# Optimization experiments

Measured on AMD Instinct MI355X. Metric: run time of the kernel, lower is better.

Reference implementation:

```python
import jax, jax.numpy as jnp
import numpy as np

MEMORY_SIZE = 32768
FEATURE_DIM = 128
BATCH = 4096


def setup_inputs() -> dict:
    key = jax.random.key(0)
    k1, k2, k3, k4 = jax.random.split(key, 4)
    memory = jax.random.normal(k1, (MEMORY_SIZE, FEATURE_DIM), dtype=jnp.float32)
    input_data = jax.random.normal(k2, (BATCH, FEATURE_DIM), dtype=jnp.float32)
    write_weights = jax.random.uniform(k3, (BATCH, MEMORY_SIZE), dtype=jnp.float32)
    query = jax.random.normal(k4, (BATCH, FEATURE_DIM), dtype=jnp.float32)
    return {"memory": memory, "input_data": input_data,
            "write_weights": write_weights, "query": query}


def reference(memory, input_data, write_weights, query):
    # ---- write(): row-normalize weights, scatter-accumulate into memory ----
    # The original python double-loop computes update[j] += w[i,j] * x[i],
    # i.e. update = w_norm.T @ x  -- a single GEMM.
    w_norm = write_weights / jnp.sum(write_weights, axis=1, keepdims=True)
    update = jnp.einsum('bm,bf->mf', w_norm, input_data)  # [M, F]
    memory_new = memory + update

    # ---- read(): softmax attention over memory slots ----
    scores = jnp.matmul(query, memory_new.T)              # [B, M]
    attention_weights = jax.nn.softmax(scores, axis=1)
    retrieved_memory = jnp.matmul(attention_weights, memory_new)  # [B, F]
    confidence_scores = jnp.max(attention_weights, axis=1)        # [B]
    return retrieved_memory, confidence_scores, memory_new
```

## Files before the change

kernel.cpp:

```cpp
#include <hip/hip_runtime.h>
#include <hip/hip_bf16.h>
#include <math.h>

#define MEMSZ 32768
#define FDIM  128
#define BATCH 4096

typedef float f32x4 __attribute__((ext_vector_type(4)));
typedef _Float16 f16x8 __attribute__((ext_vector_type(8)));
typedef short bf16x8 __attribute__((ext_vector_type(8)));
typedef unsigned short u16t;
typedef unsigned int u32t;

static __device__ __forceinline__ u16t f2h_bits(float f) {
    union { _Float16 h; u16t u; } c;
    c.h = (_Float16)f;
    return c.u;
}

#define GLDS16(gsrc, ldst) \
  __builtin_amdgcn_global_load_lds((const __attribute__((address_space(1))) void*)(gsrc), \
                                   (__attribute__((address_space(3))) void*)(ldst), 16, 0, 0)

__global__ __launch_bounds__(256) void k_sumT(const float* __restrict__ W,
                                              float* __restrict__ partial,
                                              unsigned char* __restrict__ WT64) {
    __shared__ __align__(16) unsigned char xs[32768];
    const int tid = threadIdx.x;
    const int bt = blockIdx.x & 63, mt = blockIdx.x >> 6;

    #pragma unroll
    for (int i = 0; i < 8; ++i) {
        const int gi = tid + i * 256;
        const int b = gi >> 5;
        const int srcoff = ((gi & 31) * 16) ^ ((b & 7) << 4);
        GLDS16((const unsigned char*)W + ((size_t)(bt * 64 + b) * MEMSZ + (size_t)mt * 128) * 4 + srcoff,
               &xs[gi * 16]);
    }
    asm volatile("s_waitcnt vmcnt(0)" ::: "memory");
    __syncthreads();

    {
        const int b = tid >> 2, q = tid & 3;
        float s = 0.f;
        #pragma unroll
        for (int j = 0; j < 8; ++j) {
            const int off = b * 512 + ((q * 128 + j * 16) ^ ((b & 7) << 4));
            const float4 v = *reinterpret_cast<const float4*>(&xs[off]);
            s += (v.x + v.y) + (v.z + v.w);
        }
        s += __shfl_xor(s, 1);
        s += __shfl_xor(s, 2);
        if (q == 0) partial[(size_t)mt * BATCH + bt * 64 + b] = s;
    }

    unsigned char* dst = WT64 + ((size_t)mt * 64 + bt) * 16384;
    #pragma unroll
    for (int k = 0; k < 4; ++k) {
        const int ci = tid + k * 256;
        const int wm = ci >> 8, mf = (ci >> 7) & 1, ks = (ci >> 6) & 1;
        const int l6 = ci & 63, g = l6 >> 4, q16 = l6 & 15;
        const int m = wm * 32 + mf * 16 + q16;
        u32t pk[4];
        #pragma unroll
        for (int h = 0; h < 4; ++h) {
            const int b0 = ks * 32 + g * 8 + 2 * h;
            const float lo = *reinterpret_cast<const float*>(
                &xs[b0 * 512 + ((m * 4) ^ ((b0 & 7) << 4))]);
            const float hi = *reinterpret_cast<const float*>(
                &xs[(b0 + 1) * 512 + ((m * 4) ^ (((b0 + 1) & 7) << 4))]);
            asm("v_cvt_pk_bf16_f32 %0, %1, %2" : "=v"(pk[h]) : "v"(lo), "v"(hi));
        }
        *reinterpret_cast<uint4*>(dst + ci * 16) = make_uint4(pk[0], pk[1], pk[2], pk[3]);
    }
}

__global__ __launch_bounds__(256) void k_inv(const float* __restrict__ partial,
                                             float* __restrict__ inv_s) {
    const int b = blockIdx.x * 256 + threadIdx.x;
    float s0 = 0.f, s1 = 0.f, s2 = 0.f, s3 = 0.f;
    for (int mt = 0; mt < 256; mt += 4) {
        s0 += partial[(size_t)mt * BATCH + b];
        s1 += partial[(size_t)(mt + 1) * BATCH + b];
        s2 += partial[(size_t)(mt + 2) * BATCH + b];
        s3 += partial[(size_t)(mt + 3) * BATCH + b];
    }
    inv_s[b] = 1.0f / ((s0 + s1) + (s2 + s3));
}

__global__ __launch_bounds__(256) void k_prep(const float* __restrict__ X,
                                              const float* __restrict__ inv_s,
                                              unsigned char* __restrict__ XT64) {
    __shared__ float xs[64][132];
    const int T = blockIdx.x;
    const int b0 = T * 64;
    const int tid = threadIdx.x;
    #pragma unroll
    for (int i = 0; i < 8; ++i) {
        const int idx = tid + i * 256;
        const int row = idx >> 5, c4 = idx & 31;
        const float s = inv_s[b0 + row];
        float4 v = *reinterpret_cast<const float4*>(&X[(size_t)(b0 + row) * FDIM + c4 * 4]);
        v.x *= s; v.y *= s; v.z *= s; v.w *= s;
        *reinterpret_cast<float4*>(&xs[row][c4 * 4]) = v;
    }
    __syncthreads();
    #pragma unroll
    for (int i = 0; i < 4; ++i) {
        const int L = tid + i * 256;
        const int fh = L >> 9, ff = (L >> 7) & 3, ks = (L >> 6) & 1, ln = L & 63;
        const int f = fh * 64 + ff * 16 + (ln & 15);
        const int bi = ks * 32 + (ln >> 4) * 8;
        u32t pk[4];
        #pragma unroll
        for (int h = 0; h < 4; ++h) {
            const float lo = xs[bi + 2 * h][f];
            const float hi = xs[bi + 2 * h + 1][f];
            asm("v_cvt_pk_bf16_f32 %0, %1, %2" : "=v"(pk[h]) : "v"(lo), "v"(hi));
        }
        *reinterpret_cast<uint4*>(XT64 + (size_t)T * 16384 + (size_t)L * 16) =
            make_uint4(pk[0], pk[1], pk[2], pk[3]);
    }
}

__global__ __launch_bounds__(512, 2) void k_update_mfma2(
    const unsigned char* __restrict__ WT64, const unsigned char* __restrict__ XT64,
    const float* __restrict__ Mem, float* __restrict__ MemNew,
    u16t* __restrict__ MemH, u16t* __restrict__ MemHT)
{
    const int tid = threadIdx.x;
    const int lane = tid & 63, w = tid >> 6;
    const int q16 = lane & 15, g = lane >> 4;
    const int wm = w >> 1, wf = w & 1;
    const int mblk = blockIdx.x * 128;

    const unsigned char* wbase = WT64 + (size_t)blockIdx.x * (64 * 16384)
                               + (size_t)(wm * 4096 + lane * 16);
    const unsigned char* xbase = XT64 + (size_t)(wf * 8192 + lane * 16);

    f32x4 acc[2][4];
    #pragma unroll
    for (int mf = 0; mf < 2; ++mf)
        #pragma unroll
        for (int ff = 0; ff < 4; ++ff) acc[mf][ff] = (f32x4){0.f, 0.f, 0.f, 0.f};

    auto issue = [&](bf16x8 (&ar)[2][2], bf16x8 (&br)[4][2], int t) {
        const unsigned char* wp = wbase + (size_t)t * 16384;
        #pragma unroll
        for (int mf = 0; mf < 2; ++mf)
            #pragma unroll
            for (int ks = 0; ks < 2; ++ks)
                ar[mf][ks] = *reinterpret_cast<const bf16x8*>(wp + mf * 2048 + ks * 1024);
        const unsigned char* xp = xbase + (size_t)t * 16384;
        #pragma unroll
        for (int ff = 0; ff < 4; ++ff)
            #pragma unroll
            for (int ks = 0; ks < 2; ++ks)
                br[ff][ks] = *reinterpret_cast<const bf16x8*>(xp + ff * 2048 + ks * 1024);
    };
    auto compute = [&](bf16x8 (&ar)[2][2], bf16x8 (&br)[4][2]) {
        #pragma unroll
        for (int mf = 0; mf < 2; ++mf)
            #pragma unroll
            for (int ff = 0; ff < 4; ++ff)
                #pragma unroll
                for (int ks = 0; ks < 2; ++ks)
                    acc[mf][ff] = __builtin_amdgcn_mfma_f32_16x16x32_bf16(
                        ar[mf][ks], br[ff][ks], acc[mf][ff], 0, 0, 0);
    };

    bf16x8 aE[2][2], bE[4][2], aO[2][2], bO[4][2];
    issue(aE, bE, 0); issue(aO, bO, 1);
    const int NT = BATCH / 64;
    for (int t = 0; t < NT; t += 2) {
        compute(aE, bE);
        if (t + 2 < NT) issue(aE, bE, t + 2);
        compute(aO, bO);
        if (t + 3 < NT) issue(aO, bO, t + 3);
    }

    #pragma unroll
    for (int mf = 0; mf < 2; ++mf) {
        #pragma unroll
        for (int ff = 0; ff < 4; ++ff) {
            const int m0 = mblk + wm * 32 + mf * 16 + g * 4;
            const int fcol = wf * 64 + ff * 16 + q16;
            ushort4 ht;
            u16t* htp = reinterpret_cast<u16t*>(&ht);
            #pragma unroll
            for (int r = 0; r < 4; ++r) {
                const size_t idx = (size_t)(m0 + r) * FDIM + fcol;
                const float v = acc[mf][ff][r] + Mem[idx];
                MemNew[idx] = v;
                const u16t hb = f2h_bits(v);
                MemH[idx] = hb;
                htp[r] = hb;
            }
            *reinterpret_cast<ushort4*>(&MemHT[(size_t)fcol * MEMSZ + m0]) = ht;
        }
    }
}

__global__ __launch_bounds__(256) void k_attn_mfma(
    const float* __restrict__ Q, const u16t* __restrict__ Kh, const u16t* __restrict__ KhT,
    float* __restrict__ accP, float* __restrict__ mP, float* __restrict__ lP, int s_shift)
{
    __shared__ __align__(16) unsigned char kv_u8[2][16384];
    __shared__ __align__(16) unsigned char v_u8[2][16384];
    __shared__ __align__(16) unsigned char p_u8[4][2048];

    const int tid = threadIdx.x;
    const int w = tid >> 6, lane = tid & 63;
    const int q16 = lane & 15, g = lane >> 4;
    const int S = 1 << s_shift;
    const int s_idx = blockIdx.x & (S - 1);
    const int qb = blockIdx.x >> s_shift;
    const int chunk = MEMSZ >> s_shift;
    const int slot0 = s_idx * chunk;
    const int NT = chunk >> 6;

    f16x8 qfrag[2][4];
    #pragma unroll
    for (int qf = 0; qf < 2; ++qf) {
        const float* qrow = Q + (size_t)(qb * 128 + w * 32 + qf * 16 + q16) * FDIM;
        #pragma unroll
        for (int ks = 0; ks < 4; ++ks) {
            float tmp[8];
            *reinterpret_cast<float4*>(&tmp[0]) = *reinterpret_cast<const float4*>(&qrow[ks * 32 + g * 8]);
            *reinterpret_cast<float4*>(&tmp[4]) = *reinterpret_cast<const float4*>(&qrow[ks * 32 + g * 8 + 4]);
            f16x8 v;
            #pragma unroll
            for (int e = 0; e < 8; ++e) v[e] = (_Float16)tmp[e];
            qfrag[qf][ks] = v;
        }
    }

    auto stage = [&](int buf, int tile) {
        const unsigned char* kbase = (const unsigned char*)Kh + (size_t)(slot0 + tile * 64) * 256;
        const unsigned char* tbase = (const unsigned char*)KhT + (size_t)(slot0 + tile * 64) * 2;
        #pragma unroll
        for (int c = 0; c < 4; ++c) {
            const int C = w * 4 + c;
            const int pp = C * 1024 + lane * 16;
            {
                const int slot = pp >> 8;
                const int inner = (pp & 255) ^ ((slot & 7) << 4);
                GLDS16(kbase + slot * 256 + inner, &kv_u8[buf][C * 1024]);
            }
            {
                const int d = pp >> 7;
                const int inner = (pp & 127) ^ ((d & 7) << 4);
                GLDS16(tbase + (size_t)d * 65536 + inner, &v_u8[buf][C * 1024]);
            }
        }
    };

    float m_run[2] = {-3.0e38f, -3.0e38f};
    float l_run[2] = {0.f, 0.f};
    f32x4 acc_o[8][2];
    #pragma unroll
    for (int df = 0; df < 8; ++df)
        #pragma unroll
        for (int qf = 0; qf < 2; ++qf)
            acc_o[df][qf] = (f32x4){0.f, 0.f, 0.f, 0.f};

    stage(0, 0);
    asm volatile("s_waitcnt vmcnt(0)" ::: "memory");
    __builtin_amdgcn_s_barrier();
    __builtin_amdgcn_sched_barrier(0);

    int cur = 0;
    for (int t = 0; t < NT; ++t) {
        if (t + 1 < NT) stage(cur ^ 1, t + 1);

        f32x4 acc_s[4][2];
        #pragma unroll
        for (int sf = 0; sf < 4; ++sf) {
            acc_s[sf][0] = (f32x4){0.f, 0.f, 0.f, 0.f};
            acc_s[sf][1] = (f32x4){0.f, 0.f, 0.f, 0.f};
        }
        const unsigned char* kvb = &kv_u8[cur][0];
        #pragma unroll
        for (int ks = 0; ks < 4; ++ks) {
            #pragma unroll
            for (int sf = 0; sf < 4; ++sf) {
                const int slot = sf * 16 + q16;
                const f16x8 a = *reinterpret_cast<const f16x8*>(
                    kvb + slot * 256 + ((ks * 64 + g * 16) ^ ((slot & 7) << 4)));
                acc_s[sf][0] = __builtin_amdgcn_mfma_f32_16x16x32_f16(a, qfrag[0][ks], acc_s[sf][0], 0, 0, 0);
                acc_s[sf][1] = __builtin_amdgcn_mfma_f32_16x16x32_f16(a, qfrag[1][ks], acc_s[sf][1], 0, 0, 0);
            }
        }

        f16x8 pb[2][2];
        unsigned char* pw = &p_u8[w][0];
        #pragma unroll
        for (int qf = 0; qf < 2; ++qf) {
            float pmax = acc_s[0][qf][0];
            #pragma unroll
            for (int sf = 0; sf < 4; ++sf)
                #pragma unroll
                for (int r = 0; r < 4; ++r)
                    pmax = fmaxf(pmax, acc_s[sf][qf][r]);
            pmax = fmaxf(pmax, __shfl_xor(pmax, 16));
            pmax = fmaxf(pmax, __shfl_xor(pmax, 32));
            const float mn = fmaxf(m_run[qf], pmax);
            float p[4][4];
            float psum = 0.f;
            #pragma unroll
            for (int sf = 0; sf < 4; ++sf)
                #pragma unroll
                for (int r = 0; r < 4; ++r) {
                    p[sf][r] = __expf(acc_s[sf][qf][r] - mn);
                    psum += p[sf][r];
                }
            psum += __shfl_xor(psum, 16);
            psum += __shfl_xor(psum, 32);
            const float sc = __expf(m_run[qf] - mn);
            l_run[qf] = l_run[qf] * sc + psum;
            m_run[qf] = mn;
            #pragma unroll
            for (int df = 0; df < 8; ++df) {
                acc_o[df][qf][0] *= sc; acc_o[df][qf][1] *= sc;
                acc_o[df][qf][2] *= sc; acc_o[df][qf][3] *= sc;
            }
            #pragma unroll
            for (int sf = 0; sf < 4; ++sf)
                #pragma unroll
                for (int rr = 0; rr < 2; ++rr) {
                    const u32t val = (u32t)f2h_bits(p[sf][2 * rr]) | ((u32t)f2h_bits(p[sf][2 * rr + 1]) << 16);
                    const int byte = q16 * 128 + (((sf * 16 + g * 4 + 2 * rr) * 2) ^ ((q16 & 7) << 4));
                    *reinterpret_cast<u32t*>(pw + byte) = val;
                }
            #pragma unroll
            for (int kk = 0; kk < 2; ++kk) {
                const int byte = q16 * 128 + (((kk * 32 + g * 8) * 2) ^ ((q16 & 7) << 4));
                pb[qf][kk] = *reinterpret_cast<const f16x8*>(pw + byte);
            }
        }

        const unsigned char* vb = &v_u8[cur][0];
        #pragma unroll
        for (int df = 0; df < 8; ++df) {
            #pragma unroll
            for (int kk = 0; kk < 2; ++kk) {
                const int d = df * 16 + q16;
                const f16x8 av = *reinterpret_cast<const f16x8*>(
                    vb + d * 128 + ((kk * 64 + g * 16) ^ ((d & 7) << 4)));
                acc_o[df][0] = __builtin_amdgcn_mfma_f32_16x16x32_f16(av, pb[0][kk], acc_o[df][0], 0, 0, 0);
                acc_o[df][1] = __builtin_amdgcn_mfma_f32_16x16x32_f16(av, pb[1][kk], acc_o[df][1], 0, 0, 0);
            }
        }

        asm volatile("s_waitcnt vmcnt(0)" ::: "memory");
        __builtin_amdgcn_s_barrier();
        __builtin_amdgcn_sched_barrier(0);
        cur ^= 1;
    }

    const int rowbase = qb * 128 + w * 32;
    #pragma unroll
    for (int qf = 0; qf < 2; ++qf) {
        const int row = rowbase + qf * 16 + q16;
        float* ap = accP + ((size_t)s_idx * BATCH + row) * FDIM;
        #pragma unroll
        for (int df = 0; df < 8; ++df) {
            float4 o = {acc_o[df][qf][0], acc_o[df][qf][1], acc_o[df][qf][2], acc_o[df][qf][3]};
            *reinterpret_cast<float4*>(&ap[df * 16 + g * 4]) = o;
        }
        if (g == 0) {
            mP[(size_t)s_idx * BATCH + row] = m_run[qf];
            lP[(size_t)s_idx * BATCH + row] = l_run[qf];
        }
    }
}

__global__ __launch_bounds__(256) void k_combine(const float* __restrict__ mP,
                                                 const float* __restrict__ lP,
                                                 const float* __restrict__ accP,
                                                 float* __restrict__ Out,
                                                 float* __restrict__ Conf, int S) {
    const int row = blockIdx.x * 8 + (threadIdx.x >> 5);
    const int lane = threadIdx.x & 31;
    float mt = -3.0e38f;
    for (int s = 0; s < S; ++s) mt = fmaxf(mt, mP[(size_t)s * BATCH + row]);
    float lt = 0.f;
    for (int s = 0; s < S; ++s) lt += lP[(size_t)s * BATCH + row] * __expf(mP[(size_t)s * BATCH + row] - mt);
    const float inv = 1.0f / lt;
    float4 o = {0.f, 0.f, 0.f, 0.f};
    for (int s = 0; s < S; ++s) {
        const float wgt = __expf(mP[(size_t)s * BATCH + row] - mt);
        const float4 a = *reinterpret_cast<const float4*>(&accP[((size_t)s * BATCH + row) * FDIM + lane * 4]);
        o.x += wgt * a.x; o.y += wgt * a.y; o.z += wgt * a.z; o.w += wgt * a.w;
    }
    float4 res = {o.x * inv, o.y * inv, o.z * inv, o.w * inv};
    *reinterpret_cast<float4*>(&Out[(size_t)row * FDIM + lane * 4]) = res;
    if (lane == 0) Conf[row] = inv;
}

__global__ __launch_bounds__(256) void k_rowsum(const float* __restrict__ W,
                                                float* __restrict__ inv_s) {
    const int row = blockIdx.x;
    const float4* Wr = reinterpret_cast<const float4*>(W + (size_t)row * MEMSZ);
    float acc = 0.f;
    #pragma unroll 4
    for (int i = threadIdx.x; i < MEMSZ / 4; i += 256) {
        float4 v = Wr[i];
        acc += (v.x + v.y) + (v.z + v.w);
    }
    #pragma unroll
    for (int off = 32; off > 0; off >>= 1)
        acc += __shfl_down(acc, off, 64);
    __shared__ float wsum[4];
    const int lane = threadIdx.x & 63, wid = threadIdx.x >> 6;
    if (lane == 0) wsum[wid] = acc;
    __syncthreads();
    if (threadIdx.x == 0)
        inv_s[row] = 1.0f / (wsum[0] + wsum[1] + wsum[2] + wsum[3]);
}

#define K2_IT 16
#define K2_MT 64
__global__ __launch_bounds__(256) void k_update_f32(const float* __restrict__ W,
                                                    const float* __restrict__ X,
                                                    const float* __restrict__ inv_s,
                                                    const float* __restrict__ Mem,
                                                    float* __restrict__ MemNew) {
    __shared__ float w_lds[2][K2_IT][K2_MT];
    __shared__ float x_lds[2][K2_IT][FDIM];
    const int j0 = blockIdx.x * K2_MT;
    const int tid = threadIdx.x;
    const int tf = tid & 15;
    const int tj = tid >> 4;

    float acc[4][8];
    #pragma unroll
    for (int a = 0; a < 4; ++a)
        #pragma unroll
        for (int b = 0; b < 8; ++b) acc[a][b] = 0.f;

    float4 pw, px0, px1;
    float ps0, ps1;
    const int wr = tid >> 4, wc4 = tid & 15;
    const int xr0 = tid >> 5, xc0 = tid & 31;
    const int xr1 = (tid + 256) >> 5, xc1 = tid & 31;

    auto load_tile = [&](int it) {
        const int i0 = it * K2_IT;
        pw  = *reinterpret_cast<const float4*>(&W[(size_t)(i0 + wr) * MEMSZ + j0 + wc4 * 4]);
        px0 = *reinterpret_cast<const float4*>(&X[(size_t)(i0 + xr0) * FDIM + xc0 * 4]);
        ps0 = inv_s[i0 + xr0];
        px1 = *reinterpret_cast<const float4*>(&X[(size_t)(i0 + xr1) * FDIM + xc1 * 4]);
        ps1 = inv_s[i0 + xr1];
    };
    auto write_tile = [&](int buf) {
        *reinterpret_cast<float4*>(&w_lds[buf][wr][wc4 * 4]) = pw;
        float4 v = px0; v.x *= ps0; v.y *= ps0; v.z *= ps0; v.w *= ps0;
        *reinterpret_cast<float4*>(&x_lds[buf][xr0][xc0 * 4]) = v;
        float4 u = px1; u.x *= ps1; u.y *= ps1; u.z *= ps1; u.w *= ps1;
        *reinterpret_cast<float4*>(&x_lds[buf][xr1][xc1 * 4]) = u;
    };

    load_tile(0);
    write_tile(0);
    __syncthreads();
    const int NT = BATCH / K2_IT;
    for (int it = 0; it < NT; ++it) {
        const int cur = it & 1;
        if (it + 1 < NT) load_tile(it + 1);
        #pragma unroll 4
        for (int i = 0; i < K2_IT; ++i) {
            const float4 wv = *reinterpret_cast<const float4*>(&w_lds[cur][i][tj * 4]);
            const float4 xa = *reinterpret_cast<const float4*>(&x_lds[cur][i][tf * 4]);
            const float4 xb = *reinterpret_cast<const float4*>(&x_lds[cur][i][tf * 4 + 64]);
            const float wj[4] = {wv.x, wv.y, wv.z, wv.w};
            #pragma unroll
            for (int a = 0; a < 4; ++a) {
                acc[a][0] += wj[a] * xa.x; acc[a][1] += wj[a] * xa.y;
                acc[a][2] += wj[a] * xa.z; acc[a][3] += wj[a] * xa.w;
                acc[a][4] += wj[a] * xb.x; acc[a][5] += wj[a] * xb.y;
                acc[a][6] += wj[a] * xb.z; acc[a][7] += wj[a] * xb.w;
            }
        }
        if (it + 1 < NT) write_tile(cur ^ 1);
        __syncthreads();
    }
    #pragma unroll
    for (int a = 0; a < 4; ++a) {
        const size_t j = (size_t)j0 + tj * 4 + a;
        const float4 m0 = *reinterpret_cast<const float4*>(&Mem[j * FDIM + tf * 4]);
        const float4 m1 = *reinterpret_cast<const float4*>(&Mem[j * FDIM + tf * 4 + 64]);
        float4 o0 = {acc[a][0] + m0.x, acc[a][1] + m0.y, acc[a][2] + m0.z, acc[a][3] + m0.w};
        float4 o1 = {acc[a][4] + m1.x, acc[a][5] + m1.y, acc[a][6] + m1.z, acc[a][7] + m1.w};
        *reinterpret_cast<float4*>(&MemNew[j * FDIM + tf * 4]) = o0;
        *reinterpret_cast<float4*>(&MemNew[j * FDIM + tf * 4 + 64]) = o1;
    }
}

#define QT 16
#define MT 64
#define LSTR (FDIM + 4)
__global__ __launch_bounds__(256) void k_attn_f32(const float* __restrict__ Q,
                                                  const float* __restrict__ MemNew,
                                                  float* __restrict__ Out,
                                                  float* __restrict__ Conf) {
    __shared__ float mem_lds[MT][LSTR];
    __shared__ float q_lds[QT][LSTR];
    __shared__ float p_lds[QT][MT];
    __shared__ float m_lds[QT], l_lds[QT], scale_lds[QT];

    const int tid = threadIdx.x;
    const int qblk = blockIdx.x * QT;

    #pragma unroll
    for (int r = 0; r < 2; ++r) {
        const int idx = tid + r * 256;
        const int row = idx >> 5, c4 = idx & 31;
        *reinterpret_cast<float4*>(&q_lds[row][c4 * 4]) =
            *reinterpret_cast<const float4*>(&Q[(size_t)(qblk + row) * FDIM + c4 * 4]);
    }
    if (tid < QT) { m_lds[tid] = -3.0e38f; l_lds[tid] = 0.f; }

    const int sq = (tid >> 5) * 2;
    const int sm = tid & 31;
    const int pq = tid >> 4;
    const int pf = (tid & 15) * 4;

    float acc[8];
    #pragma unroll
    for (int e = 0; e < 8; ++e) acc[e] = 0.f;

    for (int mt = 0; mt < MEMSZ / MT; ++mt) {
        __syncthreads();
        const float* src = MemNew + (size_t)mt * MT * FDIM;
        #pragma unroll
        for (int r = 0; r < 8; ++r) {
            const int idx = tid + r * 256;
            const int row = idx >> 5, c4 = idx & 31;
            *reinterpret_cast<float4*>(&mem_lds[row][c4 * 4]) =
                *reinterpret_cast<const float4*>(&src[(size_t)row * FDIM + c4 * 4]);
        }
        const float mold0 = m_lds[sq], mold1 = m_lds[sq + 1];
        __syncthreads();

        float s00 = 0.f, s01 = 0.f, s10 = 0.f, s11 = 0.f;
        #pragma unroll 8
        for (int k = 0; k < FDIM; k += 4) {
            const float4 qa = *reinterpret_cast<const float4*>(&q_lds[sq][k]);
            const float4 qb = *reinterpret_cast<const float4*>(&q_lds[sq + 1][k]);
            const float4 ma = *reinterpret_cast<const float4*>(&mem_lds[sm][k]);
            const float4 mb = *reinterpret_cast<const float4*>(&mem_lds[sm + 32][k]);
            s00 += qa.x*ma.x + qa.y*ma.y + qa.z*ma.z + qa.w*ma.w;
            s01 += qa.x*mb.x + qa.y*mb.y + qa.z*mb.z + qa.w*mb.w;
            s10 += qb.x*ma.x + qb.y*ma.y + qb.z*ma.z + qb.w*ma.w;
            s11 += qb.x*mb.x + qb.y*mb.y + qb.z*mb.z + qb.w*mb.w;
        }
        float r0 = fmaxf(s00, s01), r1 = fmaxf(s10, s11);
        #pragma unroll
        for (int off = 1; off <= 16; off <<= 1) {
            r0 = fmaxf(r0, __shfl_xor(r0, off, 64));
            r1 = fmaxf(r1, __shfl_xor(r1, off, 64));
        }
        const float mn0 = fmaxf(mold0, r0), mn1 = fmaxf(mold1, r1);
        const float p00 = __expf(s00 - mn0), p01 = __expf(s01 - mn0);
        const float p10 = __expf(s10 - mn1), p11 = __expf(s11 - mn1);
        float t0 = p00 + p01, t1 = p10 + p11;
        #pragma unroll
        for (int off = 1; off <= 16; off <<= 1) {
            t0 += __shfl_xor(t0, off, 64);
            t1 += __shfl_xor(t1, off, 64);
        }
        p_lds[sq][sm]      = p00; p_lds[sq][sm + 32]     = p01;
        p_lds[sq + 1][sm]  = p10; p_lds[sq + 1][sm + 32] = p11;
        if (sm == 0) {
            const float sc0 = __expf(mold0 - mn0), sc1 = __expf(mold1 - mn1);
            m_lds[sq] = mn0; m_lds[sq + 1] = mn1;
            l_lds[sq]     = l_lds[sq]     * sc0 + t0;
            l_lds[sq + 1] = l_lds[sq + 1] * sc1 + t1;
            scale_lds[sq] = sc0; scale_lds[sq + 1] = sc1;
        }
        __syncthreads();

        const float sc = scale_lds[pq];
        #pragma unroll
        for (int e = 0; e < 8; ++e) acc[e] *= sc;
        #pragma unroll 8
        for (int m = 0; m < MT; ++m) {
            const float p = p_lds[pq][m];
            const float4 va = *reinterpret_cast<const float4*>(&mem_lds[m][pf]);
            const float4 vb = *reinterpret_cast<const float4*>(&mem_lds[m][pf + 64]);
            acc[0] += p * va.x; acc[1] += p * va.y; acc[2] += p * va.z; acc[3] += p * va.w;
            acc[4] += p * vb.x; acc[5] += p * vb.y; acc[6] += p * vb.z; acc[7] += p * vb.w;
        }
    }
    const float linv = 1.0f / l_lds[pq];
    float4 o0 = {acc[0]*linv, acc[1]*linv, acc[2]*linv, acc[3]*linv};
    float4 o1 = {acc[4]*linv, acc[5]*linv, acc[6]*linv, acc[7]*linv};
    *reinterpret_cast<float4*>(&Out[(size_t)(qblk + pq) * FDIM + pf]) = o0;
    *reinterpret_cast<float4*>(&Out[(size_t)(qblk + pq) * FDIM + pf + 64]) = o1;
    if (tid < QT) Conf[qblk + tid] = 1.0f / l_lds[tid];
}

extern "C" void kernel_launch(void* const* d_in, const int* in_sizes, int n_in,
                              void* d_out, int out_size, void* d_ws, size_t ws_size,
                              hipStream_t stream) {
    (void)in_sizes; (void)n_in; (void)out_size;
    const float* memory   = (const float*)d_in[0];
    const float* input    = (const float*)d_in[1];
    const float* wweights = (const float*)d_in[2];
    const float* query    = (const float*)d_in[3];

    float* out       = (float*)d_out;
    float* retrieved = out;
    float* conf      = out + (size_t)BATCH * FDIM;
    float* mem_new   = conf + BATCH;

    char* ws = (char*)d_ws;
    float* inv_s = (float*)ws;

    const size_t off_xt   = 16384;
    const size_t off_part = off_xt + ((size_t)FDIM * BATCH * 2);
    const size_t off_h    = off_part + ((size_t)256 * BATCH * 4);
    const size_t off_hT   = off_h + ((size_t)MEMSZ * FDIM * 2);
    const size_t off_pc   = off_hT + ((size_t)MEMSZ * FDIM * 2);
    const size_t sz_pc    = (size_t)16 * ((size_t)BATCH * 8 + (size_t)BATCH * FDIM * 4);
    const size_t off_wt   = off_pc + sz_pc;
    const size_t need     = off_wt + (size_t)64 * 256 * 16384;

    if (ws_size >= need) {
        unsigned char* xt64 = (unsigned char*)(ws + off_xt);
        float* part = (float*)(ws + off_part);
        u16t* mh    = (u16t*)(ws + off_h);
        u16t* mhT   = (u16t*)(ws + off_hT);
        float* mP   = (float*)(ws + off_pc);
        float* lP   = mP + (size_t)16 * BATCH;
        float* accP = lP + (size_t)16 * BATCH;
        unsigned char* wt64 = (unsigned char*)(ws + off_wt);

        k_sumT<<<64 * 256, 256, 0, stream>>>(wweights, part, wt64);
        k_inv<<<BATCH / 256, 256, 0, stream>>>(part, inv_s);
        k_prep<<<BATCH / 64, 256, 0, stream>>>(input, inv_s, xt64);
        k_update_mfma2<<<MEMSZ / 128, 512, 0, stream>>>(wt64, xt64, memory, mem_new, mh, mhT);
        k_attn_mfma<<<(BATCH / 128) * 16, 256, 0, stream>>>(query, mh, mhT, accP, mP, lP, 4);
        k_combine<<<BATCH / 8, 256, 0, stream>>>(mP, lP, accP, retrieved, conf, 16);
    } else {
        k_rowsum<<<BATCH, 256, 0, stream>>>(wweights, inv_s);
        k_update_f32<<<MEMSZ / K2_MT, 256, 0, stream>>>(wweights, input, inv_s, memory, mem_new);
        k_attn_f32<<<BATCH / QT, 256, 0, stream>>>(query, mem_new, retrieved, conf);
    }
}
```

Measured before the change: 478.4 us.

## Replace LDS-staged weight transpose with register-direct pass and split update blocks

The weight-normalization pass no longer stages 64x128 tiles through LDS. Each thread now reads float4 columns straight from global memory for eight batch rows at a time, reduces row sums with wavefront shuffles and LDS atomics, and writes packed bf16 in the MFMA layout directly from registers. Each block covers 64 rows by 1024 columns, so there are 32 partial sums per row instead of 256, which shrinks the partial buffer and the k_inv reduction. The update GEMM is split into twice as many 256-thread blocks, each holding half the M tile, to give more parallelism and scheduling flexibility at the cost of reading the XT operand twice as often.

```diff
diff --git a/kernel.cpp b/kernel.cpp
--- a/kernel.cpp
+++ b/kernel.cpp
@@ -22,70 +22,71 @@
   __builtin_amdgcn_global_load_lds((const __attribute__((address_space(1))) void*)(gsrc), \
                                    (__attribute__((address_space(3))) void*)(ldst), 16, 0, 0)
 
-__global__ __launch_bounds__(256) void k_sumT(const float* __restrict__ W,
-                                              float* __restrict__ partial,
-                                              unsigned char* __restrict__ WT64) {
-    __shared__ __align__(16) unsigned char xs[32768];
+__global__ __launch_bounds__(256) void k_wpass(const float* __restrict__ W,
+                                               float* __restrict__ partial,
+                                               unsigned char* __restrict__ WT64) {
+    __shared__ float red[64];
     const int tid = threadIdx.x;
-    const int bt = blockIdx.x & 63, mt = blockIdx.x >> 6;
-
-    #pragma unroll
-    for (int i = 0; i < 8; ++i) {
-        const int gi = tid + i * 256;
-        const int b = gi >> 5;
-        const int srcoff = ((gi & 31) * 16) ^ ((b & 7) << 4);
-        GLDS16((const unsigned char*)W + ((size_t)(bt * 64 + b) * MEMSZ + (size_t)mt * 128) * 4 + srcoff,
-               &xs[gi * 16]);
-    }
-    asm volatile("s_waitcnt vmcnt(0)" ::: "memory");
+    const int bt = blockIdx.x >> 5, mseg = blockIdx.x & 31;
+    const int m0 = mseg * 1024 + tid * 4;
+    const int mt = m0 >> 7, mloc = m0 & 127;
+    const int wm = mloc >> 5, mf = (mloc >> 4) & 1, q16 = mloc & 15;
+    unsigned char* dstT = WT64 + ((size_t)mt * 64 + bt) * 16384
+                        + wm * 4096 + mf * 2048 + q16 * 16;
+    if (tid < 64) red[tid] = 0.f;
     __syncthreads();
-
-    {
-        const int b = tid >> 2, q = tid & 3;
-        float s = 0.f;
-        #pragma unroll
-        for (int j = 0; j < 8; ++j) {
-            const int off = b * 512 + ((q * 128 + j * 16) ^ ((b & 7) << 4));
-            const float4 v = *reinterpret_cast<const float4*>(&xs[off]);
-            s += (v.x + v.y) + (v.z + v.w);
-        }
-        s += __shfl_xor(s, 1);
-        s += __shfl_xor(s, 2);
-        if (q == 0) partial[(size_t)mt * BATCH + bt * 64 + b] = s;
-    }
-
-    unsigned char* dst = WT64 + ((size_t)mt * 64 + bt) * 16384;
-    #pragma unroll
-    for (int k = 0; k < 4; ++k) {
-        const int ci = tid + k * 256;
-        const int wm = ci >> 8, mf = (ci >> 7) & 1, ks = (ci >> 6) & 1;
-        const int l6 = ci & 63, g = l6 >> 4, q16 = l6 & 15;
-        const int m = wm * 32 + mf * 16 + q16;
-        u32t pk[4];
-        #pragma unroll
-        for (int h = 0; h < 4; ++h) {
-            const int b0 = ks * 32 + g * 8 + 2 * h;
-            const float lo = *reinterpret_cast<const float*>(
-                &xs[b0 * 512 + ((m * 4) ^ ((b0 & 7) << 4))]);
-            const float hi = *reinterpret_cast<const float*>(
-                &xs[(b0 + 1) * 512 + ((m * 4) ^ (((b0 + 1) & 7) << 4))]);
-            asm("v_cvt_pk_bf16_f32 %0, %1, %2" : "=v"(pk[h]) : "v"(lo), "v"(hi));
-        }
-        *reinterpret_cast<uint4*>(dst + ci * 16) = make_uint4(pk[0], pk[1], pk[2], pk[3]);
-    }
+    const int lane = tid & 63;
+
+    #pragma unroll
+    for (int ko = 0; ko < 8; ++ko) {
+        const int brow = bt * 64 + ko * 8;
+        float4 f4[8];
+        #pragma unroll
+        for (int e = 0; e < 8; ++e)
+            f4[e] = *reinterpret_cast<const float4*>(&W[(size_t)(brow + e) * MEMSZ + m0]);
+
+        float s[8];
+        #pragma unroll
+        for (int e = 0; e < 8; ++e)
+            s[e] = (f4[e].x + f4[e].y) + (f4[e].z + f4[e].w);
+        #pragma unroll
+        for (int e = 0; e < 8; ++e)
+            #pragma unroll
+            for (int off = 1; off < 64; off <<= 1)
+                s[e] += __shfl_xor(s[e], off, 64);
+        if (lane == 0) {
+            #pragma unroll
+            for (int e = 0; e < 8; ++e)
+                atomicAdd(&red[ko * 8 + e], s[e]);
+        }
+
+        unsigned char* dk = dstT + (ko >> 2) * 1024 + (ko & 3) * 256;
+        #pragma unroll
+        for (int j = 0; j < 4; ++j) {
+            float v[8];
+            #pragma unroll
+            for (int e = 0; e < 8; ++e) {
+                const float4 t4 = f4[e];
+                v[e] = (j == 0) ? t4.x : (j == 1) ? t4.y : (j == 2) ? t4.z : t4.w;
+            }
+            u32t pk[4];
+            #pragma unroll
+            for (int h = 0; h < 4; ++h)
+                asm("v_cvt_pk_bf16_f32 %0, %1, %2" : "=v"(pk[h]) : "v"(v[2 * h]), "v"(v[2 * h + 1]));
+            *reinterpret_cast<uint4*>(dk + j * 16) = make_uint4(pk[0], pk[1], pk[2], pk[3]);
+        }
+    }
+    __syncthreads();
+    if (tid < 64) partial[(size_t)mseg * BATCH + bt * 64 + tid] = red[tid];
 }
 
 __global__ __launch_bounds__(256) void k_inv(const float* __restrict__ partial,
                                              float* __restrict__ inv_s) {
     const int b = blockIdx.x * 256 + threadIdx.x;
-    float s0 = 0.f, s1 = 0.f, s2 = 0.f, s3 = 0.f;
-    for (int mt = 0; mt < 256; mt += 4) {
-        s0 += partial[(size_t)mt * BATCH + b];
-        s1 += partial[(size_t)(mt + 1) * BATCH + b];
-        s2 += partial[(size_t)(mt + 2) * BATCH + b];
-        s3 += partial[(size_t)(mt + 3) * BATCH + b];
-    }
-    inv_s[b] = 1.0f / ((s0 + s1) + (s2 + s3));
+    float s = 0.f;
+    #pragma unroll
+    for (int ms = 0; ms < 32; ++ms) s += partial[(size_t)ms * BATCH + b];
+    inv_s[b] = 1.0f / s;
 }
 
 __global__ __launch_bounds__(256) void k_prep(const float* __restrict__ X,
@@ -123,7 +124,7 @@
     }
 }
 
-__global__ __launch_bounds__(512, 2) void k_update_mfma2(
+__global__ __launch_bounds__(256) void k_update_mfma3(
     const unsigned char* __restrict__ WT64, const unsigned char* __restrict__ XT64,
     const float* __restrict__ Mem, float* __restrict__ MemNew,
     u16t* __restrict__ MemH, u16t* __restrict__ MemHT)
@@ -131,12 +132,12 @@
     const int tid = threadIdx.x;
     const int lane = tid & 63, w = tid >> 6;
     const int q16 = lane & 15, g = lane >> 4;
-    const int wm = w >> 1, wf = w & 1;
-    const int mblk = blockIdx.x * 128;
-
-    const unsigned char* wbase = WT64 + (size_t)blockIdx.x * (64 * 16384)
-                               + (size_t)(wm * 4096 + lane * 16);
-    const unsigned char* xbase = XT64 + (size_t)(wf * 8192 + lane * 16);
+    const int wm = ((blockIdx.x & 1) << 1) | (w >> 1);
+    const int wf = w & 1;
+    const int mt = blockIdx.x >> 1;
+
+    const unsigned char* wbase = WT64 + (size_t)mt * (64 * 16384) + wm * 4096 + lane * 16;
+    const unsigned char* xbase = XT64 + wf * 8192 + lane * 16;
 
     f32x4 acc[2][4];
     #pragma unroll
@@ -183,7 +184,7 @@
     for (int mf = 0; mf < 2; ++mf) {
         #pragma unroll
         for (int ff = 0; ff < 4; ++ff) {
-            const int m0 = mblk + wm * 32 + mf * 16 + g * 4;
+            const int m0 = mt * 128 + wm * 32 + mf * 16 + g * 4;
             const int fcol = wf * 64 + ff * 16 + q16;
             ushort4 ht;
             u16t* htp = reinterpret_cast<u16t*>(&ht);
@@ -620,12 +621,12 @@
 
     const size_t off_xt   = 16384;
     const size_t off_part = off_xt + ((size_t)FDIM * BATCH * 2);
-    const size_t off_h    = off_part + ((size_t)256 * BATCH * 4);
+    const size_t off_h    = off_part + ((size_t)32 * BATCH * 4);
     const size_t off_hT   = off_h + ((size_t)MEMSZ * FDIM * 2);
     const size_t off_pc   = off_hT + ((size_t)MEMSZ * FDIM * 2);
     const size_t sz_pc    = (size_t)16 * ((size_t)BATCH * 8 + (size_t)BATCH * FDIM * 4);
     const size_t off_wt   = off_pc + sz_pc;
-    const size_t need     = off_wt + (size_t)64 * 256 * 16384;
+    const size_t need     = off_wt + (size_t)256 * 64 * 16384;
 
     if (ws_size >= need) {
         unsigned char* xt64 = (unsigned char*)(ws + off_xt);
@@ -637,10 +638,10 @@
         float* accP = lP + (size_t)16 * BATCH;
         unsigned char* wt64 = (unsigned char*)(ws + off_wt);
 
-        k_sumT<<<64 * 256, 256, 0, stream>>>(wweights, part, wt64);
+        k_wpass<<<64 * 32, 256, 0, stream>>>(wweights, part, wt64);
         k_inv<<<BATCH / 256, 256, 0, stream>>>(part, inv_s);
         k_prep<<<BATCH / 64, 256, 0, stream>>>(input, inv_s, xt64);
-        k_update_mfma2<<<MEMSZ / 128, 512, 0, stream>>>(wt64, xt64, memory, mem_new, mh, mhT);
+        k_update_mfma3<<<(MEMSZ / 128) * 2, 256, 0, stream>>>(wt64, xt64, memory, mem_new, mh, mhT);
         k_attn_mfma<<<(BATCH / 128) * 16, 256, 0, stream>>>(query, mh, mhT, accP, mP, lP, 4);
         k_combine<<<BATCH / 8, 256, 0, stream>>>(mP, lP, accP, retrieved, conf, 16);
     } else {
```

After: 467.3 us. -2.3%, faster.
